# Performance work log

Hardware: AMD Instinct MI355X
Metric: run time of the kernel (lower is better)

## Reference

```python
import jax, jax.numpy as jnp
import numpy as np

B, T, C, H = 8, 1024, 768, 12
D = C // H  # head_dim = 64

def _rope_tables(seq_len, d, base=10000.0):
    inv_freq = 1.0 / (base ** (jnp.arange(0, d, 2, dtype=jnp.float32) / d))  # [d/2]
    freqs = jnp.outer(jnp.arange(seq_len, dtype=jnp.float32), inv_freq)      # [T, d/2]
    return jnp.cos(freqs), jnp.sin(freqs)

def _apply_rotary(x, cos, sin):
    # x: [B,T,H,D]; cos/sin: [1,T,1,D/2]
    d = x.shape[-1] // 2
    x1, x2 = x[..., :d], x[..., d:]
    return jnp.concatenate([x1 * cos + x2 * sin, -x1 * sin + x2 * cos], axis=-1)

def setup_inputs() -> dict:
    key = jax.random.key(0)
    k1, k2, k3 = jax.random.split(key, 3)
    x = jax.random.normal(k1, (B, T, C), dtype=jnp.float32)
    w_qkv = jax.random.normal(k2, (3 * C, C), dtype=jnp.float32) * (C ** -0.5)
    w_proj = jax.random.normal(k3, (C, C), dtype=jnp.float32) * (C ** -0.5)
    return {"x": x, "w_qkv": w_qkv, "w_proj": w_proj}

def reference(x, w_qkv, w_proj):
    Bb, Tt, Cc = x.shape
    qkv = x @ w_qkv.T                                   # [B,T,3C]
    q, k, v = jnp.split(qkv, 3, axis=2)
    q = q.reshape(Bb, Tt, H, D)
    k = k.reshape(Bb, Tt, H, D)
    v = v.reshape(Bb, Tt, H, D)
    cos, sin = _rope_tables(Tt, D)
    cos = cos[None, :, None, :]
    sin = sin[None, :, None, :]
    q = _apply_rotary(q, cos, sin)
    k = _apply_rotary(k, cos, sin)
    scale = 1.0 / jnp.sqrt(jnp.float32(D))
    scores = jnp.einsum('bthd,bshd->bhts', q, k) * scale  # [B,H,T,T]
    causal = jnp.tril(jnp.ones((Tt, Tt), dtype=bool))
    scores = jnp.where(causal[None, None], scores, jnp.finfo(scores.dtype).min)
    p = jax.nn.softmax(scores, axis=-1)
    y = jnp.einsum('bhts,bshd->bthd', p, v).reshape(Bb, Tt, Cc)
    return y @ w_proj.T
```

## Files before the change

kernel.cpp:

```cpp
#include <hip/hip_runtime.h>
#include <hip/hip_bf16.h>

#define Bb 8
#define Tt 1024
#define Cc 768
#define Hh 12
#define Dd 64
#define M_ROWS (Bb * Tt)
#define QKV_N (3 * Cc)

typedef __attribute__((ext_vector_type(8))) short s16x8;
typedef __attribute__((ext_vector_type(4))) short s16x4;
typedef __attribute__((ext_vector_type(4))) float f32x4;

static __device__ __forceinline__ short f2bf(float f) {
    union { float f; unsigned u; } v; v.f = f;
    unsigned r = (v.u + 0x7fffu + ((v.u >> 16) & 1u)) >> 16;
    return (short)r;
}

static __device__ __forceinline__ void cast8(const float* __restrict__ in,
                                             short* __restrict__ out, int i) {
    const float4 a = ((const float4*)in)[i * 2];
    const float4 b = ((const float4*)in)[i * 2 + 1];
    s16x8 f;
    f[0] = f2bf(a.x); f[1] = f2bf(a.y); f[2] = f2bf(a.z); f[3] = f2bf(a.w);
    f[4] = f2bf(b.x); f[5] = f2bf(b.y); f[6] = f2bf(b.z); f[7] = f2bf(b.w);
    ((s16x8*)out)[i] = f;
}

#define S1 (M_ROWS * Cc / 8)
#define S2 (QKV_N * Cc / 8)
#define S3 (Cc * Cc / 8)
#define SROPE (Tt * 32)
#define PREP_THREADS (S1 + S2 + S3 + SROPE)

__global__ __launch_bounds__(256) void prep_kernel(const float* __restrict__ x,
                                                   const float* __restrict__ wqkv,
                                                   const float* __restrict__ wproj,
                                                   short* __restrict__ xb,
                                                   short* __restrict__ wqkvb,
                                                   short* __restrict__ wprojb,
                                                   float2* __restrict__ cs) {
    int idx = blockIdx.x * blockDim.x + threadIdx.x;
    if (idx < S1) { cast8(x, xb, idx); return; }
    idx -= S1;
    if (idx < S2) { cast8(wqkv, wqkvb, idx); return; }
    idx -= S2;
    if (idx < S3) { cast8(wproj, wprojb, idx); return; }
    idx -= S3;
    {
        int t = idx >> 5, i = idx & 31;
        float inv_freq = exp2f(-0.41524101186092037f * (float)i);
        float fr = (float)t * inv_freq;
        float2 v; v.x = cosf(fr); v.y = sinf(fr);
        cs[idx] = v;
    }
}

template <int MODE>
__global__ __launch_bounds__(256) void gemm_nt_mfma(const short* __restrict__ A,
                                                    const short* __restrict__ B,
                                                    void* __restrict__ Cout,
                                                    const float2* __restrict__ cs,
                                                    int M, int N, int K, int nblocks) {
    __shared__ short As[128 * 64];
    __shared__ short Bs[128 * 64];

    const int wave = threadIdx.x >> 6;
    const int lane = threadIdx.x & 63;
    const int l16  = lane & 15;
    const int quad = lane >> 4;
    const int wm = (wave >> 1) * 64;
    const int wn = (wave & 1) * 64;

    const int mb8  = (M >> 7) >> 3;
    const int xcd  = blockIdx.x & 7;
    const int slot = blockIdx.x >> 3;
    const int bm = (xcd * mb8 + slot / nblocks) * 128;
    const int bn = (slot % nblocks) * 128;

    f32x4 acc[4][4] = {};

    for (int k0 = 0; k0 < K; k0 += 64) {
        __syncthreads();
#pragma unroll
        for (int j = 0; j < 4; j++) {
            const int idx = (j * 4 + wave) * 64 + lane;
            const int row = idx >> 3;
            const int kc  = (((idx & 7) ^ ((idx >> 3) & 7)) * 8);
            __builtin_amdgcn_global_load_lds(
                (const __attribute__((address_space(1))) unsigned*)
                    (A + (size_t)(bm + row) * K + k0 + kc),
                (__attribute__((address_space(3))) unsigned*)&As[(j * 4 + wave) * 512],
                16, 0, 0);
            __builtin_amdgcn_global_load_lds(
                (const __attribute__((address_space(1))) unsigned*)
                    (B + (size_t)(bn + row) * K + k0 + kc),
                (__attribute__((address_space(3))) unsigned*)&Bs[(j * 4 + wave) * 512],
                16, 0, 0);
        }
        __syncthreads();

#pragma unroll
        for (int c = 0; c < 2; c++) {
            const int swz = (l16 & 7) * 8;
            const int col = (c * 32 + quad * 8) ^ swz;
            s16x8 af[4], bfr[4];
#pragma unroll
            for (int mt = 0; mt < 4; mt++)
                af[mt] = *(const s16x8*)&As[(wm + mt * 16 + l16) * 64 + col];
#pragma unroll
            for (int nt = 0; nt < 4; nt++)
                bfr[nt] = *(const s16x8*)&Bs[(wn + nt * 16 + l16) * 64 + col];
#pragma unroll
            for (int mt = 0; mt < 4; mt++)
#pragma unroll
                for (int nt = 0; nt < 4; nt++)
                    acc[mt][nt] = __builtin_amdgcn_mfma_f32_16x16x32_bf16(
                        af[mt], bfr[nt], acc[mt][nt], 0, 0, 0);
        }
    }

    if constexpr (MODE == 0) {
#pragma unroll
        for (int mt = 0; mt < 4; mt++)
#pragma unroll
            for (int r = 0; r < 4; r++) {
                const size_t row = bm + wm + mt * 16 + quad * 4 + r;
#pragma unroll
                for (int nt = 0; nt < 4; nt++)
                    ((float*)Cout)[row * N + bn + wn + nt * 16 + l16] = acc[mt][nt][r];
            }
    } else {
        const bool is_v = (bn >= 2 * Cc);
        if (is_v) {
#pragma unroll
            for (int mt = 0; mt < 4; mt++)
#pragma unroll
                for (int r = 0; r < 4; r++) {
                    const size_t row = bm + wm + mt * 16 + quad * 4 + r;
#pragma unroll
                    for (int nt = 0; nt < 4; nt++)
                        ((short*)Cout)[row * N + bn + wn + nt * 16 + l16] = f2bf(acc[mt][nt][r]);
                }
        } else {
            const float scale = (bn < Cc) ? 0.125f : 1.0f;
#pragma unroll
            for (int mt = 0; mt < 4; mt++) {
#pragma unroll
                for (int r = 0; r < 4; r++) {
                    const int row = bm + wm + mt * 16 + quad * 4 + r;
                    const int t = row & (Tt - 1);
                    const float2 c0 = cs[t * 32 + l16];
                    const float2 c1 = cs[t * 32 + 16 + l16];
                    const float x0 = acc[mt][0][r], x1 = acc[mt][1][r];
                    const float x2 = acc[mt][2][r], x3 = acc[mt][3][r];
                    short* cp = (short*)Cout + (size_t)row * N + bn + wn;
                    cp[l16]      = f2bf((x0 * c0.x + x2 * c0.y) * scale);
                    cp[16 + l16] = f2bf((x1 * c1.x + x3 * c1.y) * scale);
                    cp[32 + l16] = f2bf((-x0 * c0.y + x2 * c0.x) * scale);
                    cp[48 + l16] = f2bf((-x1 * c1.y + x3 * c1.x) * scale);
                }
            }
        }
    }
}

#define KSP 72
#define VSP 72
#define PP  76

__global__ __launch_bounds__(256) void flash_attn(const short* __restrict__ qkv,
                                                  short* __restrict__ y) {
    __shared__ short Ks[2][64 * KSP];
    __shared__ short Vs[2][Dd * VSP];
    __shared__ short Ps[4][16 * PP];

    const int wave = threadIdx.x >> 6;
    const int lane = threadIdx.x & 63;
    const int l16  = lane & 15;
    const int quad = lane >> 4;

    const int pair = blockIdx.x / 96;
    const int bh   = blockIdx.x % 96;
    const int h = bh % Hh;
    const int b = bh / Hh;
    const int qa_blk = pair;
    const int qb_blk = 15 - pair;
    const int q0a = qa_blk * 64 + wave * 16;
    const int q0b = qb_blk * 64 + wave * 16;

    s16x8 qfa[2], qfb[2];
    {
        const short* qpa = qkv + (size_t)(b * Tt + q0a + l16) * QKV_N + h * Dd + quad * 8;
        const short* qpb = qkv + (size_t)(b * Tt + q0b + l16) * QKV_N + h * Dd + quad * 8;
        qfa[0] = *(const s16x8*)qpa;  qfa[1] = *(const s16x8*)(qpa + 32);
        qfb[0] = *(const s16x8*)qpb;  qfb[1] = *(const s16x8*)(qpb + 32);
    }

    f32x4 oa[4] = {}, ob[4] = {};
    float la[4] = {0.f, 0.f, 0.f, 0.f}, lb[4] = {0.f, 0.f, 0.f, 0.f};

    short* pw = &Ps[wave][0];

    const int krow = threadIdx.x >> 2;
    const int kd0  = (threadIdx.x & 3) * 16;
    const int key2 = (threadIdx.x & 31) * 2;
    const int dv0  = (threadIdx.x >> 5) * 8;

    s16x8 pk0, pk1, pv0, pv1;
    auto load_tile = [&](int kbase) {
        const short* kp = qkv + (size_t)(b * Tt + kbase + krow) * QKV_N + Cc + h * Dd + kd0;
        pk0 = *(const s16x8*)kp;
        pk1 = *(const s16x8*)(kp + 8);
        const short* vp = qkv + (size_t)(b * Tt + kbase + key2) * QKV_N + 2 * Cc + h * Dd + dv0;
        pv0 = *(const s16x8*)vp;
        pv1 = *(const s16x8*)(vp + QKV_N);
    };
    auto store_tile = [&](int buf) {
        *(s16x8*)&Ks[buf][krow * KSP + kd0]     = pk0;
        *(s16x8*)&Ks[buf][krow * KSP + kd0 + 8] = pk1;
#pragma unroll
        for (int j = 0; j < 8; j++) {
            ushort2 w; w.x = (unsigned short)pv0[j]; w.y = (unsigned short)pv1[j];
            *(ushort2*)&Vs[buf][(dv0 + j) * VSP + key2] = w;
        }
    };

    auto process = [&](int buf, int q0, const s16x8* qf, f32x4* o, float* l_r,
                       int kbase, bool masked) {
        f32x4 sv[4];
#pragma unroll
        for (int g = 0; g < 4; g++) {
            s16x8 kf0 = *(const s16x8*)&Ks[buf][(g * 16 + l16) * KSP + quad * 8];
            s16x8 kf1 = *(const s16x8*)&Ks[buf][(g * 16 + l16) * KSP + 32 + quad * 8];
            f32x4 z = {};
            z = __builtin_amdgcn_mfma_f32_16x16x32_bf16(qf[0], kf0, z, 0, 0, 0);
            z = __builtin_amdgcn_mfma_f32_16x16x32_bf16(qf[1], kf1, z, 0, 0, 0);
            sv[g] = z;
        }
#pragma unroll
        for (int r = 0; r < 4; r++) {
            const int qg = q0 + quad * 4 + r;
            float rs = 0.f;
#pragma unroll
            for (int g = 0; g < 4; g++) {
                float p = __expf(sv[g][r]);
                if (masked) p = (kbase + g * 16 + l16 <= qg) ? p : 0.0f;
                rs += p;
                pw[(quad * 4 + r) * PP + g * 16 + l16] = f2bf(p);
            }
            l_r[r] += rs;
        }
#pragma unroll
        for (int c = 0; c < 2; c++) {
            s16x4 plo = *(const s16x4*)&pw[l16 * PP + c * 32 + quad * 8];
            s16x4 phi = *(const s16x4*)&pw[l16 * PP + c * 32 + quad * 8 + 4];
            s16x8 pa = __builtin_shufflevector(plo, phi, 0, 1, 2, 3, 4, 5, 6, 7);
#pragma unroll
            for (int nc = 0; nc < 4; nc++) {
                s16x8 vb = *(const s16x8*)&Vs[buf][(nc * 16 + l16) * VSP + c * 32 + quad * 8];
                o[nc] = __builtin_amdgcn_mfma_f32_16x16x32_bf16(pa, vb, o[nc], 0, 0, 0);
            }
        }
    };

    load_tile(0);
    store_tile(0);
    for (int kt = 0; kt <= qb_blk; kt++) {
        __syncthreads();
        const int nb = (kt < qb_blk) ? (kt + 1) * 64 : qb_blk * 64;
        load_tile(nb);
        const int buf = kt & 1;
        const int kbase = kt * 64;
        process(buf, q0b, qfb, ob, lb, kbase, kt == qb_blk);
        if (kt <= qa_blk)
            process(buf, q0a, qfa, oa, la, kbase, kt == qa_blk);
        store_tile(buf ^ 1);
    }

#pragma unroll
    for (int r = 0; r < 4; r++) {
        float sa = la[r], sb = lb[r];
#pragma unroll
        for (int off = 1; off < 16; off <<= 1) {
            sa += __shfl_xor(sa, off, 64);
            sb += __shfl_xor(sb, off, 64);
        }
        const float inva = 1.0f / sa;
        const float invb = 1.0f / sb;
        short* ypa = y + (size_t)(b * Tt + q0a + quad * 4 + r) * Cc + h * Dd;
        short* ypb = y + (size_t)(b * Tt + q0b + quad * 4 + r) * Cc + h * Dd;
#pragma unroll
        for (int nc = 0; nc < 4; nc++) {
            ypa[nc * 16 + l16] = f2bf(oa[nc][r] * inva);
            ypb[nc * 16 + l16] = f2bf(ob[nc][r] * invb);
        }
    }
}

extern "C" void kernel_launch(void* const* d_in, const int* in_sizes, int n_in,
                              void* d_out, int out_size, void* d_ws, size_t ws_size,
                              hipStream_t stream) {
    const float* x      = (const float*)d_in[0];
    const float* w_qkv  = (const float*)d_in[1];
    const float* w_proj = (const float*)d_in[2];
    float* out = (float*)d_out;

    float2* cs    = (float2*)d_ws;
    short* xb     = (short*)(cs + Tt * 32);
    short* wqkvb  = xb + (size_t)M_ROWS * Cc;
    short* wprojb = wqkvb + (size_t)QKV_N * Cc;
    short* qkvb   = wprojb + (size_t)Cc * Cc;
    short* yb     = qkvb + (size_t)M_ROWS * QKV_N;

    prep_kernel<<<PREP_THREADS / 256, 256, 0, stream>>>(
        x, w_qkv, w_proj, xb, wqkvb, wprojb, cs);

    gemm_nt_mfma<1><<<(QKV_N / 128) * (M_ROWS / 128), 256, 0, stream>>>(
        xb, wqkvb, qkvb, cs, M_ROWS, QKV_N, Cc, QKV_N / 128);

    flash_attn<<<96 * 8, 256, 0, stream>>>(qkvb, yb);

    gemm_nt_mfma<0><<<(Cc / 128) * (M_ROWS / 128), 256, 0, stream>>>(
        yb, wprojb, out, nullptr, M_ROWS, Cc, Cc, Cc / 128);
}
```

Before: 187.7 us.

## Double-buffer GEMM LDS tiles with K-step 32 and new swizzle

Splits the GEMM shared-memory tiles into two buffers of half depth (K=32) and issues the global-to-LDS loads for the next K-slice before computing on the current one. This aims to overlap memory latency with MFMA work and removes one of the two barriers per iteration. The LDS layout and XOR swizzle are redone for the 32-wide tiles. The risk is that only one barrier per iteration may not fully order the async LDS writes against reads of the other buffer, and the shorter K step doubles the number of iterations and barriers.

New measurement: 185.1 us. No clear change (-1.4%).

```diff
diff --git a/kernel.cpp b/kernel.cpp
--- a/kernel.cpp
+++ b/kernel.cpp
@@ -12,6 +12,9 @@
 typedef __attribute__((ext_vector_type(8))) short s16x8;
 typedef __attribute__((ext_vector_type(4))) short s16x4;
 typedef __attribute__((ext_vector_type(4))) float f32x4;
+
+#define AS1 __attribute__((address_space(1)))
+#define AS3 __attribute__((address_space(3)))
 
 static __device__ __forceinline__ short f2bf(float f) {
     union { float f; unsigned u; } v; v.f = f;
@@ -64,8 +67,8 @@
                                                     void* __restrict__ Cout,
                                                     const float2* __restrict__ cs,
                                                     int M, int N, int K, int nblocks) {
-    __shared__ short As[128 * 64];
-    __shared__ short Bs[128 * 64];
+    __shared__ short As[2][128 * 32];
+    __shared__ short Bs[2][128 * 32];
 
     const int wave = threadIdx.x >> 6;
     const int lane = threadIdx.x & 63;
@@ -82,44 +85,49 @@
 
     f32x4 acc[4][4] = {};
 
-    for (int k0 = 0; k0 < K; k0 += 64) {
+    auto stage = [&](int k0, int buf) {
+#pragma unroll
+        for (int j = 0; j < 2; j++) {
+            const int D = (j * 4 + wave) * 64 + lane;
+            const int G = D >> 3;
+            const int s = (G << 3) | ((D & 7) ^ (G & 7));
+            const int m  = s >> 2;
+            const int c4 = (s & 3) * 8;
+            __builtin_amdgcn_global_load_lds(
+                (const AS1 unsigned*)(A + (size_t)(bm + m) * K + k0 + c4),
+                (AS3 unsigned*)&As[buf][(j * 4 + wave) * 512], 16, 0, 0);
+            __builtin_amdgcn_global_load_lds(
+                (const AS1 unsigned*)(B + (size_t)(bn + m) * K + k0 + c4),
+                (AS3 unsigned*)&Bs[buf][(j * 4 + wave) * 512], 16, 0, 0);
+        }
+    };
+
+    const int nIter = K >> 5;
+    stage(0, 0);
+    for (int kt = 0; kt < nIter; kt++) {
+        const int buf = kt & 1;
         __syncthreads();
-#pragma unroll
-        for (int j = 0; j < 4; j++) {
-            const int idx = (j * 4 + wave) * 64 + lane;
-            const int row = idx >> 3;
-            const int kc  = (((idx & 7) ^ ((idx >> 3) & 7)) * 8);
-            __builtin_amdgcn_global_load_lds(
-                (const __attribute__((address_space(1))) unsigned*)
-                    (A + (size_t)(bm + row) * K + k0 + kc),
-                (__attribute__((address_space(3))) unsigned*)&As[(j * 4 + wave) * 512],
-                16, 0, 0);
-            __builtin_amdgcn_global_load_lds(
-                (const __attribute__((address_space(1))) unsigned*)
-                    (B + (size_t)(bn + row) * K + k0 + kc),
-                (__attribute__((address_space(3))) unsigned*)&Bs[(j * 4 + wave) * 512],
-                16, 0, 0);
-        }
-        __syncthreads();
-
-#pragma unroll
-        for (int c = 0; c < 2; c++) {
-            const int swz = (l16 & 7) * 8;
-            const int col = (c * 32 + quad * 8) ^ swz;
-            s16x8 af[4], bfr[4];
-#pragma unroll
-            for (int mt = 0; mt < 4; mt++)
-                af[mt] = *(const s16x8*)&As[(wm + mt * 16 + l16) * 64 + col];
+        if (kt + 1 < nIter) stage((kt + 1) << 5, buf ^ 1);
+
+        s16x8 af[4], bfr[4];
+#pragma unroll
+        for (int mt = 0; mt < 4; mt++) {
+            const int m = wm + mt * 16 + l16;
+            const int d = (4 * (m & 1) + quad) ^ ((m >> 1) & 7);
+            af[mt] = *(const s16x8*)&As[buf][(m >> 1) * 64 + d * 8];
+        }
+#pragma unroll
+        for (int nt = 0; nt < 4; nt++) {
+            const int n = wn + nt * 16 + l16;
+            const int d = (4 * (n & 1) + quad) ^ ((n >> 1) & 7);
+            bfr[nt] = *(const s16x8*)&Bs[buf][(n >> 1) * 64 + d * 8];
+        }
+#pragma unroll
+        for (int mt = 0; mt < 4; mt++)
 #pragma unroll
             for (int nt = 0; nt < 4; nt++)
-                bfr[nt] = *(const s16x8*)&Bs[(wn + nt * 16 + l16) * 64 + col];
-#pragma unroll
-            for (int mt = 0; mt < 4; mt++)
-#pragma unroll
-                for (int nt = 0; nt < 4; nt++)
-                    acc[mt][nt] = __builtin_amdgcn_mfma_f32_16x16x32_bf16(
-                        af[mt], bfr[nt], acc[mt][nt], 0, 0, 0);
-        }
+                acc[mt][nt] = __builtin_amdgcn_mfma_f32_16x16x32_bf16(
+                    af[mt], bfr[nt], acc[mt][nt], 0, 0, 0);
     }
 
     if constexpr (MODE == 0) {
```
